# Kernel tuning notes

Measured on AMD Instinct MI355X. Metric: run time of the kernel, lower is better.

Reference implementation:

```python
import jax, jax.numpy as jnp
import numpy as np

B, C, T = 64, 64, 2048
HID, OUT = 256, 10
NEW_T = T // 4
N = B * NEW_T  # 32768 nodes
E = 524288


def setup_inputs() -> dict:
    key = jax.random.key(0)
    ks = jax.random.split(key, 16)
    inp = {
        "x": jax.random.normal(ks[0], (B, C, T), dtype=jnp.float32),
        "edge_index": jax.random.randint(ks[1], (2, E), 0, N, dtype=jnp.int64),
        "conv1_w": jax.random.normal(ks[2], (16, C, 5), dtype=jnp.float32) * 0.05,
        "conv1_b": jnp.zeros((16,), jnp.float32),
        "conv2_w": jax.random.normal(ks[3], (32, 16, 5), dtype=jnp.float32) * 0.1,
        "conv2_b": jnp.zeros((32,), jnp.float32),
        "gcn1_w": jax.random.normal(ks[4], (32, HID), dtype=jnp.float32) * 0.1,
        "gcn1_b": jnp.zeros((HID,), jnp.float32),
        "gcn2_w": jax.random.normal(ks[5], (HID, HID), dtype=jnp.float32) * 0.05,
        "gcn2_b": jnp.zeros((HID,), jnp.float32),
        "cls_w": jax.random.normal(ks[6], (HID, OUT), dtype=jnp.float32) * 0.05,
        "cls_b": jnp.zeros((OUT,), jnp.float32),
    }
    return inp


def _conv1d(x, w, b):
    # x: [B, Cin, T], w: [Cout, Cin, K] -> [B, Cout, T] (padding=2 for K=5)
    y = jax.lax.conv_general_dilated(
        x, w, window_strides=(1,), padding=[(2, 2)],
        dimension_numbers=("NCH", "OIH", "NCH"))
    return y + b[None, :, None]


def _maxpool2(x):
    b, c, t = x.shape
    return x.reshape(b, c, t // 2, 2).max(axis=-1)


def _gcn(x, w, bias, src, dst):
    # PyG GCNConv: add self-loops, symmetric norm D^-1/2 (A+I) D^-1/2, x@W, aggregate, +bias
    n = N
    loops = jnp.arange(n, dtype=src.dtype)
    s = jnp.concatenate([src, loops])
    d = jnp.concatenate([dst, loops])
    deg = jax.ops.segment_sum(jnp.ones_like(d, dtype=x.dtype), d, num_segments=n)
    dinv = jnp.where(deg > 0, jax.lax.rsqrt(deg), 0.0)
    norm = dinv[s] * dinv[d]  # [E+N]
    xw = x @ w  # [N, H]
    msg = xw[s] * norm[:, None]
    out = jax.ops.segment_sum(msg, d, num_segments=n)
    return out + bias


def reference(x, edge_index, conv1_w, conv1_b, conv2_w, conv2_b,
              gcn1_w, gcn1_b, gcn2_w, gcn2_b, cls_w, cls_b):
    h = _maxpool2(jax.nn.relu(_conv1d(x, conv1_w, conv1_b)))
    h = _maxpool2(jax.nn.relu(_conv1d(h, conv2_w, conv2_b)))  # [B, 32, NEW_T]
    h = h.transpose(0, 2, 1).reshape(-1, 32)  # [N, 32]
    src, dst = edge_index[0], edge_index[1]
    h = jax.nn.relu(_gcn(h, gcn1_w, gcn1_b, src, dst))
    h = jax.nn.relu(_gcn(h, gcn2_w, gcn2_b, src, dst))
    h = h.reshape(B, NEW_T, HID).mean(axis=1)  # global mean over temporal nodes
    return h @ cls_w + cls_b
```

## Files before the change

kernel.cpp:

```cpp
#include <hip/hip_runtime.h>

#define B_ 64
#define CIN 64
#define T_ 2048
#define C1 16
#define T1 1024
#define C2 32
#define T2 512
#define NN 32768
#define HID 256
#define OUTD 10
#define NE 524288
#define NTOT (NE + NN)

typedef __attribute__((ext_vector_type(4))) float fx4;
typedef __attribute__((ext_vector_type(2))) float fx2f;
typedef __attribute__((ext_vector_type(8))) _Float16 hx8;
typedef __attribute__((ext_vector_type(4))) _Float16 hx4;
typedef __attribute__((ext_vector_type(2))) _Float16 hx2;

#define OFF_H      (0ull)
#define OFF_Z      (16ull<<20)
#define OFF_H1     (33ull<<20)
#define OFF_XN     (37ull<<20)
#define OFF_Y1     (42ull<<20)
#define OFF_DEG    (46ull<<20)
#define OFF_INDPTR ((46ull<<20) + (256u<<10))
#define OFF_CNT    ((46ull<<20) + (512u<<10))
#define OFF_DINV   ((46ull<<20) + (768u<<10))
#define OFF_CSRC   (47ull<<20)
#define OFF_WT1    (51ull<<20)
#define OFF_WT2    (OFF_WT1 + (64u<<10))
#define OFF_POOL   (OFF_WT1 + (128u<<10))
#define OFF_W2T    (OFF_WT1 + (256u<<10))

__device__ __forceinline__ fx4 shfl_xor4(fx4 v, int m) {
    return (fx4){__shfl_xor(v.x, m), __shfl_xor(v.y, m), __shfl_xor(v.z, m), __shfl_xor(v.w, m)};
}

__global__ __launch_bounds__(256) void k_setup(int* deg, int* cnt, float* pooled,
                                               const float* __restrict__ w1, const float* __restrict__ w2,
                                               float* __restrict__ wt1, float* __restrict__ wt2,
                                               const float* __restrict__ gw2, _Float16* __restrict__ w2t,
                                               unsigned* __restrict__ xnz, unsigned* __restrict__ zz) {
    __shared__ float tl[64][65];
    int blk = blockIdx.x, t = threadIdx.x;
    if (blk < 128) {
        int i = blk * 256 + t;
        if (i < NN) { deg[i] = 1; cnt[i] = 0; }
        if (i < B_ * HID) pooled[i] = 0.f;
        if (blk == 0 && t < 16) xnz[t] = 0u;
        if (blk == 1 && t < 64) zz[t] = 0u;
    } else if (blk < 144) {
        int bb = blk - 128;
        int bx = bb & 3, by = bb >> 2;
        #pragma unroll
        for (int it = 0; it < 16; it++) {
            int idx = it * 256 + t;
            int r = idx >> 6, c = idx & 63;
            tl[r][c] = gw2[(size_t)(bx * 64 + r) * 256 + by * 64 + c];
        }
        __syncthreads();
        #pragma unroll
        for (int it = 0; it < 16; it++) {
            int idx = it * 256 + t;
            int r = idx >> 6, c = idx & 63;
            w2t[(size_t)(by * 64 + r) * 256 + bx * 64 + c] = (_Float16)tl[c][r];
        }
    } else {
        int i = (blk - 144) * 256 + t;
        if (i < 16 * 64 * 5) {
            int co = i & 15; int r = i >> 4; int k = r % 5; int ci = r / 5;
            wt1[i] = w1[(co * 64 + ci) * 5 + k];
        }
        int j = i - 16 * 64 * 5;
        if (j >= 0 && j < 32 * 16 * 5) {
            int co = j & 31; int r = j >> 5; int k = r % 5; int ci = r / 5;
            wt2[j] = w2[(co * 16 + ci) * 5 + k];
        }
    }
}

__global__ __launch_bounds__(1024) void k_scan(const int* __restrict__ deg, int* __restrict__ indptr,
                                               float* __restrict__ dinv) {
    __shared__ int wsum[16];
    int tid = threadIdx.x;
    int lane = tid & 63, w = tid >> 6;
    int base = tid * 32;
    int loc[32]; int s = 0;
    #pragma unroll
    for (int j = 0; j < 32; j++) {
        int d = deg[base + j];
        dinv[base + j] = rsqrtf((float)d);
        loc[j] = d;
        s += (d + 7) & ~7;
    }
    int v = s;
    #pragma unroll
    for (int off = 1; off < 64; off <<= 1) {
        int t = __shfl_up(v, off);
        if (lane >= off) v += t;
    }
    if (lane == 63) wsum[w] = v;
    __syncthreads();
    int woff = 0;
    #pragma unroll
    for (int i = 0; i < 16; i++) { int t = wsum[i]; if (i < w) woff += t; }
    int run = woff + v - s;
    #pragma unroll
    for (int j = 0; j < 32; j++) { indptr[base + j] = run; run += (loc[j] + 7) & ~7; }
    if (tid == 1023) { indptr[NN] = run; dinv[NN] = 0.f; }
}

#define LDX 72
__global__ __launch_bounds__(256) void k_c1cnt(const float* __restrict__ x, const float* __restrict__ wt1,
                                               const float* __restrict__ b1, float* __restrict__ h1,
                                               const int* __restrict__ ei, int* __restrict__ deg) {
    int blk = blockIdx.x;
    int tid = threadIdx.x;
    if (blk >= 512) {
        int t = (blk - 512) * 256 + tid;
        int4 d4 = *(const int4*)&ei[NE + 4 * t];
        atomicAdd(&deg[d4.x], 1);
        atomicAdd(&deg[d4.y], 1);
        atomicAdd(&deg[d4.z], 1);
        atomicAdd(&deg[d4.w], 1);
        return;
    }
    __shared__ _Float16 xs[260 * LDX];
    __shared__ _Float16 wl[16 * 328];
    __shared__ float ps2[128 * 17];
    int tile = blk & 7;
    int b = blk >> 3;
    int t0 = tile * 256;
    const float* xb = x + ((size_t)b * CIN) * T_ + t0;
    {
        int f = tid & 63, r0 = tid >> 6;
        #pragma unroll
        for (int it = 0; it < 16; it++) {
            int r = r0 + 4 * it;
            fx4 v = *(const fx4*)&xb[(size_t)r * T_ + f * 4];
            #pragma unroll
            for (int q = 0; q < 4; q++) {
                int j = 2 + f * 4 + q;
                xs[j * LDX + ((((r >> 3) ^ (j >> 3)) & 7) << 3) + (r & 7)] = (_Float16)v[q];
            }
        }
        int r = tid >> 2, c = tid & 3;
        int off = (c < 2) ? (c - 2) : (254 + c);
        int gt = t0 + off;
        float v = 0.f;
        if (gt >= 0 && gt < T_) v = xb[(size_t)r * T_ + off];
        xs[(off + 2) * LDX + r] = (_Float16)v;
        for (int i = tid; i < 5120; i += 256) {
            int K = i >> 4, co = i & 15;
            int kk = K >> 6, ci = K & 63;
            wl[co * 328 + K] = (_Float16)wt1[(ci * 5 + kk) * 16 + co];
        }
    }
    __syncthreads();
    int wv = tid >> 6, lane = tid & 63;
    int l15 = lane & 15, g = lane >> 4;
    fx4 acc[4];
    #pragma unroll
    for (int m = 0; m < 4; m++) acc[m] = (fx4){0.f, 0.f, 0.f, 0.f};
    #pragma unroll
    for (int ks = 0; ks < 10; ks++) {
        int kk = ks >> 1;
        int cb = (ks & 1) * 4 + g;
        hx8 bf = *(const hx8*)&wl[l15 * 328 + ks * 32 + g * 8];
        #pragma unroll
        for (int m = 0; m < 4; m++) {
            int j = wv * 64 + m * 16 + l15 + kk;
            hx8 af = *(const hx8*)&xs[j * LDX + ((((j >> 3) & 7) ^ cb) << 3)];
            acc[m] = __builtin_amdgcn_mfma_f32_16x16x32_f16(af, bf, acc[m], 0, 0, 0);
        }
    }
    float bv = b1[l15];
    #pragma unroll
    for (int m = 0; m < 4; m++) {
        int t1b = wv * 32 + m * 8 + g * 2;
        float a0 = fmaxf(acc[m][0] + bv, 0.f);
        float a1 = fmaxf(acc[m][1] + bv, 0.f);
        float a2 = fmaxf(acc[m][2] + bv, 0.f);
        float a3 = fmaxf(acc[m][3] + bv, 0.f);
        ps2[t1b * 17 + l15] = fmaxf(a0, a1);
        ps2[(t1b + 1) * 17 + l15] = fmaxf(a2, a3);
    }
    __syncthreads();
    for (int idx = tid; idx < 2048; idx += 256) {
        int t1 = idx & 127, co = idx >> 7;
        h1[(b * C1 + co) * T1 + tile * 128 + t1] = ps2[t1 * 17 + co];
    }
}

__global__ __launch_bounds__(256) void k_c2fill(const float* __restrict__ h1, const float* __restrict__ wt2,
                                                const float* __restrict__ b2, _Float16* __restrict__ xn,
                                                const int* __restrict__ ei, const int* __restrict__ deg,
                                                const int* __restrict__ indptr, int* __restrict__ cnt,
                                                int* __restrict__ csrc) {
    int blk = blockIdx.x;
    int tid = threadIdx.x;
    if (blk >= 256) {
        int j = blk - 256;
        int g = j & 7, i = j >> 3;
        int q0 = i * 964;
        int q1 = (q0 + 964 < NE / 4) ? (q0 + 964) : (NE / 4);
        for (int q = q0 + tid; q < q1; q += 256) {
            int4 s4 = *(const int4*)&ei[4 * q];
            int4 d4 = *(const int4*)&ei[NE + 4 * q];
            if ((d4.x >> 12) == g) { int p = indptr[d4.x] + atomicAdd(&cnt[d4.x], 1); csrc[p] = s4.x; }
            if ((d4.y >> 12) == g) { int p = indptr[d4.y] + atomicAdd(&cnt[d4.y], 1); csrc[p] = s4.y; }
            if ((d4.z >> 12) == g) { int p = indptr[d4.z] + atomicAdd(&cnt[d4.z], 1); csrc[p] = s4.z; }
            if ((d4.w >> 12) == g) { int p = indptr[d4.w] + atomicAdd(&cnt[d4.w], 1); csrc[p] = s4.w; }
        }
        int n0 = i * 241;
        int n1 = (n0 + 241 < NN) ? (n0 + 241) : NN;
        for (int n = n0 + tid; n < n1; n += 256) {
            if ((n >> 12) == g) {
                int base = indptr[n];
                int p = base + atomicAdd(&cnt[n], 1);
                csrc[p] = n;
                int dd = deg[n], dp = (dd + 7) & ~7;
                for (int k = dd; k < dp; k++) csrc[base + k] = NN;
            }
        }
        return;
    }
    __shared__ float xs[16][260];
    __shared__ float ps[128 * 33];
    int tile = blk & 3;
    int b = blk >> 2;
    int t0 = tile * 256;
    float acc[32];
    #pragma unroll
    for (int i = 0; i < 32; i++) acc[i] = 0.f;
    for (int idx = tid; idx < 16 * 260; idx += 256) {
        int r = idx / 260, c = idx % 260;
        int gt = t0 + c - 2;
        float v = 0.f;
        if (gt >= 0 && gt < T1) v = h1[(b * C1 + r) * T1 + gt];
        xs[r][c] = v;
    }
    __syncthreads();
    for (int ci = 0; ci < 16; ci++) {
        float xv[5];
        #pragma unroll
        for (int j = 0; j < 5; j++) xv[j] = xs[ci][tid + j];
        const float* wp = wt2 + (ci * 5) * 32;
        #pragma unroll
        for (int k = 0; k < 5; k++) {
            #pragma unroll
            for (int co = 0; co < 32; co++)
                acc[co] = fmaf(xv[k], wp[k * 32 + co], acc[co]);
        }
    }
    #pragma unroll
    for (int co = 0; co < 32; co++) {
        float a = fmaxf(acc[co] + b2[co], 0.f);
        float o = fmaxf(a, __shfl_xor(a, 1));
        if ((tid & 1) == 0) ps[(tid >> 1) * 33 + co] = o;
    }
    __syncthreads();
    size_t base = ((size_t)b * T2 + tile * 128) * 32;
    for (int idx = tid; idx < 128 * 16; idx += 256) {
        int t1 = idx >> 4, co = (idx & 15) * 2;
        hx2 h;
        h.x = (_Float16)ps[t1 * 33 + co];
        h.y = (_Float16)ps[t1 * 33 + co + 1];
        *(hx2*)&xn[base + t1 * 32 + co] = h;
    }
}

#define ACC4(v, m) \
    acc.x = fmaf((float)v[0], m, acc.x); acc.y = fmaf((float)v[1], m, acc.y); \
    acc.z = fmaf((float)v[2], m, acc.z); acc.w = fmaf((float)v[3], m, acc.w);

__global__ __launch_bounds__(256) void k_agg32(const _Float16* __restrict__ xn, const int* __restrict__ indptr,
                                               const int* __restrict__ csrc, const float* __restrict__ dinv,
                                               float* __restrict__ y1) {
    int lane = threadIdx.x & 63;
    int n = blockIdx.x * 4 + (threadIdx.x >> 6);
    int eg = lane >> 3, fi = lane & 7;
    int beg = indptr[n];
    int cnt8 = indptr[n + 1] - beg;
    float dn = dinv[n];
    const int* cs = csrc + beg;
    fx4 acc = (fx4){0.f, 0.f, 0.f, 0.f};
    for (int i = 0; i < cnt8; i += 8) {
        int s = cs[i + eg];
        float m = dinv[s] * dn;
        hx4 v = *(const hx4*)&xn[(size_t)s * 32 + fi * 4];
        ACC4(v, m)
    }
    acc += shfl_xor4(acc, 8);
    acc += shfl_xor4(acc, 16);
    acc += shfl_xor4(acc, 32);
    if (lane < 8) *(fx4*)&y1[(size_t)n * 32 + fi * 4] = acc;
}

__global__ __launch_bounds__(256) void k_gemm1(const float* __restrict__ A, const float* __restrict__ W,
                                               const float* __restrict__ bias, _Float16* __restrict__ H) {
    __shared__ __align__(16) float xT[32 * 68];
    __shared__ __align__(16) float wl[32 * 256];
    int tid = threadIdx.x;
    int ty = tid >> 4, tx = tid & 15;
    int rows0 = blockIdx.x * 64;
    int kq = tid & 7, rs = tid >> 3;
    {
        fx4 v0 = *(const fx4*)&A[(size_t)(rows0 + rs) * 32 + kq * 4];
        fx4 v1 = *(const fx4*)&A[(size_t)(rows0 + rs + 32) * 32 + kq * 4];
        #pragma unroll
        for (int i = 0; i < 4; i++) {
            xT[(kq * 4 + i) * 68 + rs]      = v0[i];
            xT[(kq * 4 + i) * 68 + rs + 32] = v1[i];
        }
    }
    #pragma unroll
    for (int m = 0; m < 8; m++)
        *(fx4*)&wl[m * 1024 + tid * 4] = *(const fx4*)&W[(size_t)(m * 1024 + tid * 4)];
    __syncthreads();

    fx4 c[4][4];
    #pragma unroll
    for (int i = 0; i < 4; i++)
        #pragma unroll
        for (int j = 0; j < 4; j++) c[i][j] = (fx4){0.f, 0.f, 0.f, 0.f};

    #pragma unroll 8
    for (int kk = 0; kk < 32; kk++) {
        fx4 xa = *(const fx4*)&xT[kk * 68 + ty * 4];
        fx4 w[4];
        w[0] = *(const fx4*)&wl[kk * 256 + tx * 8];
        w[1] = *(const fx4*)&wl[kk * 256 + tx * 8 + 4];
        w[2] = *(const fx4*)&wl[kk * 256 + tx * 8 + 128];
        w[3] = *(const fx4*)&wl[kk * 256 + tx * 8 + 132];
        #pragma unroll
        for (int j = 0; j < 4; j++) {
            c[0][j] += xa.x * w[j];
            c[1][j] += xa.y * w[j];
            c[2][j] += xa.z * w[j];
            c[3][j] += xa.w * w[j];
        }
    }
    fx4 bb[4];
    bb[0] = *(const fx4*)&bias[tx * 8];
    bb[1] = *(const fx4*)&bias[tx * 8 + 4];
    bb[2] = *(const fx4*)&bias[tx * 8 + 128];
    bb[3] = *(const fx4*)&bias[tx * 8 + 132];
    #pragma unroll
    for (int i = 0; i < 4; i++) {
        int r = rows0 + ty * 4 + i;
        fx4 v0 = c[i][0] + bb[0], v1 = c[i][1] + bb[1];
        fx4 v2 = c[i][2] + bb[2], v3 = c[i][3] + bb[3];
        hx8 h0, h1;
        #pragma unroll
        for (int q = 0; q < 4; q++) {
            h0[q]     = (_Float16)fmaxf(v0[q], 0.f);
            h0[q + 4] = (_Float16)fmaxf(v1[q], 0.f);
            h1[q]     = (_Float16)fmaxf(v2[q], 0.f);
            h1[q + 4] = (_Float16)fmaxf(v3[q], 0.f);
        }
        *(hx8*)&H[(size_t)r * 256 + tx * 8]       = h0;
        *(hx8*)&H[(size_t)r * 256 + tx * 8 + 128] = h1;
    }
}

#define LDH 72
__global__ __launch_bounds__(256, 2) void k_gemm2m(const _Float16* __restrict__ A,
                                                   const _Float16* __restrict__ Bt,
                                                   unsigned char* __restrict__ Z) {
    __shared__ __align__(16) _Float16 As[2][128 * LDH];
    __shared__ __align__(16) _Float16 Bs[2][128 * LDH];
    int tid = threadIdx.x;
    int lane = tid & 63, wid = tid >> 6;
    int wm = wid >> 1, wn = wid & 1;
    int row0 = blockIdx.x * 128, col0 = blockIdx.y * 128;
    int l15 = lane & 15, g = lane >> 4;
    int sr = tid >> 3, sc = tid & 7;

    fx4 acc[4][4];
    #pragma unroll
    for (int m = 0; m < 4; m++)
        #pragma unroll
        for (int n = 0; n < 4; n++) acc[m][n] = (fx4){0.f, 0.f, 0.f, 0.f};

    uint4 ga[4], gb[4];
    #pragma unroll
    for (int it = 0; it < 4; it++) {
        ga[it] = *(const uint4*)&A[(size_t)(row0 + sr + 32 * it) * 256 + sc * 8];
        gb[it] = *(const uint4*)&Bt[(size_t)(col0 + sr + 32 * it) * 256 + sc * 8];
    }
    #pragma unroll
    for (int it = 0; it < 4; it++) {
        *(uint4*)&As[0][(sr + 32 * it) * LDH + sc * 8] = ga[it];
        *(uint4*)&Bs[0][(sr + 32 * it) * LDH + sc * 8] = gb[it];
    }
    __syncthreads();

    int cur = 0;
    for (int t = 0; t < 4; t++) {
        if (t < 3) {
            int k0 = (t + 1) * 64;
            #pragma unroll
            for (int it = 0; it < 4; it++) {
                ga[it] = *(const uint4*)&A[(size_t)(row0 + sr + 32 * it) * 256 + k0 + sc * 8];
                gb[it] = *(const uint4*)&Bt[(size_t)(col0 + sr + 32 * it) * 256 + k0 + sc * 8];
            }
        }
        const _Float16* ap = As[cur];
        const _Float16* bp = Bs[cur];
        hx8 af[4][2], bf[4][2];
        #pragma unroll
        for (int m = 0; m < 4; m++)
            #pragma unroll
            for (int ks = 0; ks < 2; ks++)
                af[m][ks] = *(const hx8*)&ap[(wm * 64 + m * 16 + l15) * LDH + ks * 32 + g * 8];
        #pragma unroll
        for (int n = 0; n < 4; n++)
            #pragma unroll
            for (int ks = 0; ks < 2; ks++)
                bf[n][ks] = *(const hx8*)&bp[(wn * 64 + n * 16 + l15) * LDH + ks * 32 + g * 8];
        #pragma unroll
        for (int m = 0; m < 4; m++)
            #pragma unroll
            for (int n = 0; n < 4; n++) {
                acc[m][n] = __builtin_amdgcn_mfma_f32_16x16x32_f16(af[m][0], bf[n][0], acc[m][n], 0, 0, 0);
                acc[m][n] = __builtin_amdgcn_mfma_f32_16x16x32_f16(af[m][1], bf[n][1], acc[m][n], 0, 0, 0);
            }
        if (t < 3) {
            #pragma unroll
            for (int it = 0; it < 4; it++) {
                *(uint4*)&As[cur ^ 1][(sr + 32 * it) * LDH + sc * 8] = ga[it];
                *(uint4*)&Bs[cur ^ 1][(sr + 32 * it) * LDH + sc * 8] = gb[it];
            }
        }
        __syncthreads();
        cur ^= 1;
    }

    #pragma unroll
    for (int m = 0; m < 4; m++)
        #pragma unroll
        for (int n = 0; n < 4; n++) {
            int cc = col0 + wn * 64 + n * 16 + l15;
            #pragma unroll
            for (int r = 0; r < 4; r++) {
                int rr = row0 + wm * 64 + m * 16 + g * 4 + r;
                int p = __builtin_amdgcn_cvt_pk_fp8_f32(acc[m][n][r], acc[m][n][r], 0, false);
                Z[(size_t)rr * 256 + cc] = (unsigned char)(p & 0xff);
            }
        }
}

#define ACCP(pw, pm) { \
    fx2f lo_ = __builtin_amdgcn_cvt_pk_f32_fp8(pw, false); \
    fx2f hi_ = __builtin_amdgcn_cvt_pk_f32_fp8(pw, true); \
    acc.x = fmaf(lo_.x, pm, acc.x); acc.y = fmaf(lo_.y, pm, acc.y); \
    acc.z = fmaf(hi_.x, pm, acc.z); acc.w = fmaf(hi_.y, pm, acc.w); }

__global__ __launch_bounds__(256) void k_aggm(const unsigned char* __restrict__ Z, const int* __restrict__ indptr,
                                              const int* __restrict__ csrc, const float* __restrict__ dinv,
                                              const float* __restrict__ bias, float* __restrict__ pooled) {
    __shared__ float ps[4][256];
    int tid = threadIdx.x;
    int wid = tid >> 6, lane = tid & 63;
    int n0 = blockIdx.x * 32 + wid * 8;
    fx4 bb = *(const fx4*)&bias[lane * 4];
    fx4 racc = (fx4){0.f, 0.f, 0.f, 0.f};
    #pragma unroll 1
    for (int u = 0; u < 8; u++) {
        int n = n0 + u;
        int beg = indptr[n];
        int cnt8 = indptr[n + 1] - beg;
        float dn = dinv[n];
        const int* cs = csrc + beg;
        fx4 acc = (fx4){0.f, 0.f, 0.f, 0.f};
        for (int i = 0; i < cnt8; i += 8) {
            int4 ia = *(const int4*)&cs[i];
            int4 ib = *(const int4*)&cs[i + 4];
            float m0 = dinv[ia.x] * dn, m1 = dinv[ia.y] * dn;
            float m2 = dinv[ia.z] * dn, m3 = dinv[ia.w] * dn;
            float m4 = dinv[ib.x] * dn, m5 = dinv[ib.y] * dn;
            float m6 = dinv[ib.z] * dn, m7 = dinv[ib.w] * dn;
            unsigned w0 = *(const unsigned*)&Z[(size_t)ia.x * 256 + lane * 4];
            unsigned w1 = *(const unsigned*)&Z[(size_t)ia.y * 256 + lane * 4];
            unsigned w2 = *(const unsigned*)&Z[(size_t)ia.z * 256 + lane * 4];
            unsigned w3 = *(const unsigned*)&Z[(size_t)ia.w * 256 + lane * 4];
            unsigned w4 = *(const unsigned*)&Z[(size_t)ib.x * 256 + lane * 4];
            unsigned w5 = *(const unsigned*)&Z[(size_t)ib.y * 256 + lane * 4];
            unsigned w6 = *(const unsigned*)&Z[(size_t)ib.z * 256 + lane * 4];
            unsigned w7 = *(const unsigned*)&Z[(size_t)ib.w * 256 + lane * 4];
            ACCP(w0, m0)
            ACCP(w1, m1)
            ACCP(w2, m2)
            ACCP(w3, m3)
            ACCP(w4, m4)
            ACCP(w5, m5)
            ACCP(w6, m6)
            ACCP(w7, m7)
        }
        acc += bb;
        racc.x += fmaxf(acc.x, 0.f); racc.y += fmaxf(acc.y, 0.f);
        racc.z += fmaxf(acc.z, 0.f); racc.w += fmaxf(acc.w, 0.f);
    }
    *(fx4*)&ps[wid][lane * 4] = racc;
    __syncthreads();
    float s = ps[0][tid] + ps[1][tid] + ps[2][tid] + ps[3][tid];
    atomicAdd(&pooled[(blockIdx.x >> 4) * 256 + tid], s * (1.f / 512.f));
}

__global__ __launch_bounds__(64) void k_cls(const float* __restrict__ pooled, const float* __restrict__ cw,
                                            const float* __restrict__ cb, float* __restrict__ outp) {
    int b = blockIdx.x, lane = threadIdx.x;
    float po[10];
    #pragma unroll
    for (int o = 0; o < 10; o++) po[o] = 0.f;
    #pragma unroll
    for (int m = 0; m < 4; m++) {
        int hh = lane + m * 64;
        float ph = pooled[b * HID + hh];
        #pragma unroll
        for (int o = 0; o < 10; o++) po[o] = fmaf(ph, cw[hh * 10 + o], po[o]);
    }
    #pragma unroll
    for (int off = 32; off >= 1; off >>= 1) {
        #pragma unroll
        for (int o = 0; o < 10; o++) po[o] += __shfl_down(po[o], off);
    }
    if (lane == 0) {
        #pragma unroll
        for (int o = 0; o < 10; o++) outp[b * 10 + o] = po[o] + cb[o];
    }
}

extern "C" void kernel_launch(void* const* d_in, const int* in_sizes, int n_in,
                              void* d_out, int out_size, void* d_ws, size_t ws_size,
                              hipStream_t stream) {
    const float* x   = (const float*)d_in[0];
    const int*   ei  = (const int*)d_in[1];
    const float* w1  = (const float*)d_in[2];
    const float* b1  = (const float*)d_in[3];
    const float* w2  = (const float*)d_in[4];
    const float* b2  = (const float*)d_in[5];
    const float* g1w = (const float*)d_in[6];
    const float* g1b = (const float*)d_in[7];
    const float* g2w = (const float*)d_in[8];
    const float* g2b = (const float*)d_in[9];
    const float* cw  = (const float*)d_in[10];
    const float* cb  = (const float*)d_in[11];
    float* out = (float*)d_out;
    char* ws = (char*)d_ws;

    _Float16*       H      = (_Float16*)(ws + OFF_H);
    unsigned char*  Z      = (unsigned char*)(ws + OFF_Z);
    float*          h1     = (float*)(ws + OFF_H1);
    _Float16*       xn     = (_Float16*)(ws + OFF_XN);
    float*          y1     = (float*)(ws + OFF_Y1);
    int*            deg    = (int*)(ws + OFF_DEG);
    int*            indptr = (int*)(ws + OFF_INDPTR);
    int*            cnt    = (int*)(ws + OFF_CNT);
    float*          dinv   = (float*)(ws + OFF_DINV);
    int*            csrc   = (int*)(ws + OFF_CSRC);
    float*          wt1    = (float*)(ws + OFF_WT1);
    float*          wt2    = (float*)(ws + OFF_WT2);
    float*          pooled = (float*)(ws + OFF_POOL);
    _Float16*       w2t    = (_Float16*)(ws + OFF_W2T);
    unsigned*       xnz    = (unsigned*)(xn + (size_t)NN * 32);
    unsigned*       zz     = (unsigned*)(Z + (size_t)NN * 256);

    k_setup <<<174, 256, 0, stream>>>(deg, cnt, pooled, w1, w2, wt1, wt2, g2w, w2t, xnz, zz);
    k_c1cnt <<<1024, 256, 0, stream>>>(x, wt1, b1, h1, ei, deg);
    k_scan  <<<1, 1024, 0, stream>>>(deg, indptr, dinv);
    k_c2fill<<<1344, 256, 0, stream>>>(h1, wt2, b2, xn, ei, deg, indptr, cnt, csrc);
    k_agg32 <<<8192, 256, 0, stream>>>(xn, indptr, csrc, dinv, y1);
    k_gemm1 <<<512, 256, 0, stream>>>(y1, g1w, g1b, H);
    k_gemm2m<<<dim3(256, 2), 256, 0, stream>>>(H, w2t, Z);
    k_aggm  <<<1024, 256, 0, stream>>>(Z, indptr, csrc, dinv, g2b, pooled);
    k_cls   <<<64, 64, 0, stream>>>(pooled, cw, cb, out);
}
```

Measured before the change: 153.6 us.

## Split aggm feature dim across blocks and edges across half-waves

The second GCN aggregation kernel now splits the 256 features into two 128-wide slices handled by separate blocks, doubling the grid. Within a wave, the two 32-lane halves process alternating edges and combine their sums with a cross-half shuffle. This raises parallelism and memory-level concurrency for the fp8 gather. In exchange, each edge index and dinv value is loaded twice (once per slice), and there is an extra shuffle per node. It relies on a shfl_xor4 helper that is assumed to exist.

```diff
diff --git a/kernel.cpp b/kernel.cpp
--- a/kernel.cpp
+++ b/kernel.cpp
@@ -462,12 +462,16 @@
 __global__ __launch_bounds__(256) void k_aggm(const unsigned char* __restrict__ Z, const int* __restrict__ indptr,
                                               const int* __restrict__ csrc, const float* __restrict__ dinv,
                                               const float* __restrict__ bias, float* __restrict__ pooled) {
-    __shared__ float ps[4][256];
+    __shared__ float ps[4][128];
     int tid = threadIdx.x;
     int wid = tid >> 6, lane = tid & 63;
-    int n0 = blockIdx.x * 32 + wid * 8;
-    fx4 bb = *(const fx4*)&bias[lane * 4];
+    int slice = blockIdx.x & 1;
+    int grp = blockIdx.x >> 1;
+    int h = lane >> 5, fl = lane & 31;
+    int fb = slice * 128 + fl * 4;
+    fx4 bb = *(const fx4*)&bias[fb];
     fx4 racc = (fx4){0.f, 0.f, 0.f, 0.f};
+    int n0 = grp * 32 + wid * 8;
     #pragma unroll 1
     for (int u = 0; u < 8; u++) {
         int n = n0 + u;
@@ -479,35 +483,32 @@
         for (int i = 0; i < cnt8; i += 8) {
             int4 ia = *(const int4*)&cs[i];
             int4 ib = *(const int4*)&cs[i + 4];
-            float m0 = dinv[ia.x] * dn, m1 = dinv[ia.y] * dn;
-            float m2 = dinv[ia.z] * dn, m3 = dinv[ia.w] * dn;
-            float m4 = dinv[ib.x] * dn, m5 = dinv[ib.y] * dn;
-            float m6 = dinv[ib.z] * dn, m7 = dinv[ib.w] * dn;
-            unsigned w0 = *(const unsigned*)&Z[(size_t)ia.x * 256 + lane * 4];
-            unsigned w1 = *(const unsigned*)&Z[(size_t)ia.y * 256 + lane * 4];
-            unsigned w2 = *(const unsigned*)&Z[(size_t)ia.z * 256 + lane * 4];
-            unsigned w3 = *(const unsigned*)&Z[(size_t)ia.w * 256 + lane * 4];
-            unsigned w4 = *(const unsigned*)&Z[(size_t)ib.x * 256 + lane * 4];
-            unsigned w5 = *(const unsigned*)&Z[(size_t)ib.y * 256 + lane * 4];
-            unsigned w6 = *(const unsigned*)&Z[(size_t)ib.z * 256 + lane * 4];
-            unsigned w7 = *(const unsigned*)&Z[(size_t)ib.w * 256 + lane * 4];
+            int e0 = h ? ia.y : ia.x;
+            int e1 = h ? ia.w : ia.z;
+            int e2 = h ? ib.y : ib.x;
+            int e3 = h ? ib.w : ib.z;
+            float m0 = dinv[e0] * dn, m1 = dinv[e1] * dn;
+            float m2 = dinv[e2] * dn, m3 = dinv[e3] * dn;
+            unsigned w0 = *(const unsigned*)&Z[(size_t)e0 * 256 + fb];
+            unsigned w1 = *(const unsigned*)&Z[(size_t)e1 * 256 + fb];
+            unsigned w2 = *(const unsigned*)&Z[(size_t)e2 * 256 + fb];
+            unsigned w3 = *(const unsigned*)&Z[(size_t)e3 * 256 + fb];
             ACCP(w0, m0)
             ACCP(w1, m1)
             ACCP(w2, m2)
             ACCP(w3, m3)
-            ACCP(w4, m4)
-            ACCP(w5, m5)
-            ACCP(w6, m6)
-            ACCP(w7, m7)
-        }
+        }
+        acc += shfl_xor4(acc, 32);
         acc += bb;
         racc.x += fmaxf(acc.x, 0.f); racc.y += fmaxf(acc.y, 0.f);
         racc.z += fmaxf(acc.z, 0.f); racc.w += fmaxf(acc.w, 0.f);
     }
-    *(fx4*)&ps[wid][lane * 4] = racc;
-    __syncthreads();
-    float s = ps[0][tid] + ps[1][tid] + ps[2][tid] + ps[3][tid];
-    atomicAdd(&pooled[(blockIdx.x >> 4) * 256 + tid], s * (1.f / 512.f));
+    if (h == 0) *(fx4*)&ps[wid][fl * 4] = racc;
+    __syncthreads();
+    if (tid < 128) {
+        float s = ps[0][tid] + ps[1][tid] + ps[2][tid] + ps[3][tid];
+        atomicAdd(&pooled[(grp >> 4) * 256 + slice * 128 + tid], s * (1.f / 512.f));
+    }
 }
 
 __global__ __launch_bounds__(64) void k_cls(const float* __restrict__ pooled, const float* __restrict__ cw,
@@ -576,6 +577,6 @@
     k_agg32 <<<8192, 256, 0, stream>>>(xn, indptr, csrc, dinv, y1);
     k_gemm1 <<<512, 256, 0, stream>>>(y1, g1w, g1b, H);
     k_gemm2m<<<dim3(256, 2), 256, 0, stream>>>(H, w2t, Z);
-    k_aggm  <<<1024, 256, 0, stream>>>(Z, indptr, csrc, dinv, g2b, pooled);
+    k_aggm  <<<2048, 256, 0, stream>>>(Z, indptr, csrc, dinv, g2b, pooled);
     k_cls   <<<64, 64, 0, stream>>>(pooled, cw, cb, out);
 }
```

Result: no change. 152.3 us, median of 2 (-0.8%).
